# Optimization experiments

Measured on AMD Instinct MI355X. Metric: run time of the kernel, lower is better.

The kernel has to match this reference:

```python
import jax, jax.numpy as jnp
import numpy as np

B, T_IN, F, NB = 32768, 3, 6, 10
H = 256
BD = H // 2            # baseline_dim
T_OUT = 5
DIN = F + H + BD       # decoder LSTMCell input size
EPS = 1e-5


def _lstm_cell(x, h, c, W_ih, W_hh, b_ih, b_hh):
    # PyTorch gate order: i, f, g, o
    z = x @ W_ih.T + h @ W_hh.T + b_ih + b_hh
    i, f, g, o = jnp.split(z, 4, axis=-1)
    c = jax.nn.sigmoid(f) * c + jax.nn.sigmoid(i) * jnp.tanh(g)
    h = jax.nn.sigmoid(o) * jnp.tanh(c)
    return h, c


def _lstm_layer(xs, W_ih, W_hh, b_ih, b_hh):
    # xs: (T, B, D_in) -> outputs (T, B, H), final (h, c)
    Bn = xs.shape[1]
    h0 = jnp.zeros((Bn, H), xs.dtype)
    c0 = jnp.zeros((Bn, H), xs.dtype)

    def step(carry, x):
        h, c = carry
        h, c = _lstm_cell(x, h, c, W_ih, W_hh, b_ih, b_hh)
        return (h, c), h

    (hT, cT), ys = jax.lax.scan(step, (h0, c0), xs)
    return ys, hT, cT


def setup_inputs() -> dict:
    key = jax.random.key(0)
    ks = jax.random.split(key, 16)
    s = 0.05
    d = {
        "cbc_input": jax.random.normal(ks[0], (B, T_IN, F), jnp.float32),
        "baseline": jax.random.normal(ks[1], (B, NB), jnp.float32),
        # encoder LSTM layer 0 / 1
        "W_ih0": jax.random.normal(ks[2], (4 * H, F), jnp.float32) * s,
        "W_hh0": jax.random.normal(ks[3], (4 * H, H), jnp.float32) * s,
        "b_ih0": jnp.zeros((4 * H,), jnp.float32),
        "b_hh0": jnp.zeros((4 * H,), jnp.float32),
        "W_ih1": jax.random.normal(ks[4], (4 * H, H), jnp.float32) * s,
        "W_hh1": jax.random.normal(ks[5], (4 * H, H), jnp.float32) * s,
        "b_ih1": jnp.zeros((4 * H,), jnp.float32),
        "b_hh1": jnp.zeros((4 * H,), jnp.float32),
        # baseline encoder: Linear + ReLU + LayerNorm
        "Wb": jax.random.normal(ks[6], (BD, NB), jnp.float32) * s,
        "bb": jnp.zeros((BD,), jnp.float32),
        "ln_g": jnp.ones((BD,), jnp.float32),
        "ln_b": jnp.zeros((BD,), jnp.float32),
        # Bahdanau attention
        "W1a": jax.random.normal(ks[7], (H, H), jnp.float32) * s,
        "b1a": jnp.zeros((H,), jnp.float32),
        "W2a": jax.random.normal(ks[8], (H, H), jnp.float32) * s,
        "b2a": jnp.zeros((H,), jnp.float32),
        "va": jax.random.normal(ks[9], (1, H), jnp.float32) * s,
        "ba": jnp.zeros((1,), jnp.float32),
        # decoder LSTMCell
        "Wd_ih": jax.random.normal(ks[10], (4 * H, DIN), jnp.float32) * s,
        "Wd_hh": jax.random.normal(ks[11], (4 * H, H), jnp.float32) * s,
        "bd_ih": jnp.zeros((4 * H,), jnp.float32),
        "bd_hh": jnp.zeros((4 * H,), jnp.float32),
        # output projection MLP
        "Wo1": jax.random.normal(ks[12], (BD, H), jnp.float32) * s,
        "bo1": jnp.zeros((BD,), jnp.float32),
        "Wo2": jax.random.normal(ks[13], (F, BD), jnp.float32) * s,
        "bo2": jnp.zeros((F,), jnp.float32),
    }
    return d


def reference(cbc_input, baseline, W_ih0, W_hh0, b_ih0, b_hh0,
              W_ih1, W_hh1, b_ih1, b_hh1, Wb, bb, ln_g, ln_b,
              W1a, b1a, W2a, b2a, va, ba,
              Wd_ih, Wd_hh, bd_ih, bd_hh, Wo1, bo1, Wo2, bo2):
    # ---- encoder (2-layer LSTM, batch_first; eval mode so no dropout) ----
    xs = jnp.swapaxes(cbc_input, 0, 1)                      # (T, B, F)
    y0, _, _ = _lstm_layer(xs, W_ih0, W_hh0, b_ih0, b_hh0)  # (T, B, H)
    y1, hT, cT = _lstm_layer(y0, W_ih1, W_hh1, b_ih1, b_hh1)
    encoder_outputs = jnp.swapaxes(y1, 0, 1)                # (B, T, H)

    # ---- baseline encoder: Linear -> ReLU -> LayerNorm ----
    z = jax.nn.relu(baseline @ Wb.T + bb)
    mu = jnp.mean(z, axis=-1, keepdims=True)
    var = jnp.mean((z - mu) ** 2, axis=-1, keepdims=True)
    baseline_repr = (z - mu) * jax.lax.rsqrt(var + EPS) * ln_g + ln_b  # (B, BD)

    enc_proj = encoder_outputs @ W2a.T + b2a                # (B, T, H) precomputed
    last_cbc0 = cbc_input[:, -1, :]                         # (B, F)

    def step(carry, _):
        h, c, last_cbc = carry
        # Bahdanau attention
        q = (h @ W1a.T + b1a)[:, None, :]                   # (B, 1, H)
        scores = jnp.tanh(q + enc_proj) @ va.T + ba         # (B, T, 1)
        weights = jax.nn.softmax(scores, axis=1)
        context = jnp.sum(weights * encoder_outputs, axis=1)  # (B, H)
        dec_in = jnp.concatenate([last_cbc, context, baseline_repr], axis=1)
        h, c = _lstm_cell(dec_in, h, c, Wd_ih, Wd_hh, bd_ih, bd_hh)
        delta = jax.nn.relu(h @ Wo1.T + bo1) @ Wo2.T + bo2
        pred = last_cbc + delta
        return (h, c, pred), pred

    _, preds = jax.lax.scan(step, (hT, cT, last_cbc0), None, length=T_OUT)
    return jnp.swapaxes(preds, 0, 1)                        # (B, 5, F)
```

## Files before the change

kernel.cpp:

```cpp
#include <hip/hip_runtime.h>

typedef unsigned short u16;
typedef __bf16 bf16x8 __attribute__((ext_vector_type(8)));
typedef float f32x4 __attribute__((ext_vector_type(4)));

#define BATCH 32768L

__device__ __forceinline__ u16 f2b(float f) {
  union { float f; unsigned int u; } v; v.f = f;
  unsigned int r = v.u + 0x7fffu + ((v.u >> 16) & 1u);
  return (u16)(r >> 16);
}
__device__ __forceinline__ float b2f(u16 h) {
  union { unsigned int u; float f; } v; v.u = ((unsigned int)h) << 16;
  return v.f;
}
__device__ __forceinline__ float sigf(float x) { return 1.f / (1.f + __expf(-x)); }
__device__ __forceinline__ float tanh_f(float x) { return 2.f / (1.f + __expf(-2.f * x)) - 1.f; }

__device__ __forceinline__ void gload16(const void* g, void* l) {
  __builtin_amdgcn_global_load_lds((const __attribute__((address_space(1))) unsigned int*)g,
                                   (__attribute__((address_space(3))) unsigned int*)l,
                                   16, 0, 0);
}

struct PrepP {
  const float* s[9]; u16* d[9]; int sc[9]; int dc[9]; long n[9];
  const float* ba[3]; const float* bb_[3]; float* bo[3];
};

__global__ void prep_kernel(PrepP p, long cvtTotal, long total) {
  for (long i = (long)blockIdx.x * blockDim.x + threadIdx.x; i < total;
       i += (long)gridDim.x * blockDim.x) {
    if (i < cvtTotal) {
      long off = i; int sg = 0;
      while (off >= p.n[sg]) { off -= p.n[sg]; ++sg; }
      long r = off / p.dc[sg]; int c = (int)(off - r * p.dc[sg]);
      p.d[sg][off] = (c < p.sc[sg]) ? f2b(p.s[sg][r * (long)p.sc[sg] + c]) : (u16)0;
    } else {
      long j = i - cvtTotal; int sg = (int)(j >> 10); int k = (int)(j & 1023);
      p.bo[sg][k] = p.ba[sg][k] + p.bb_[sg][k];
    }
  }
}

__global__ void cvt_pad_kernel(const float* __restrict__ src, u16* __restrict__ dst,
                               long rows, int scols, int dstride) {
  long n = rows * (long)dstride;
  for (long i = (long)blockIdx.x * blockDim.x + threadIdx.x; i < n;
       i += (long)gridDim.x * blockDim.x) {
    long r = i / dstride; int c = (int)(i - r * dstride);
    dst[i] = (c < scols) ? f2b(src[r * (long)scols + c]) : (u16)0;
  }
}

__global__ void init_last_kernel(const float* __restrict__ cbc, u16* __restrict__ dec_in, long n) {
  long i = (long)blockIdx.x * 256 + threadIdx.x;
  if (i < n) {
    long r = i / 6; int j = (int)(i - r * 6);
    dec_in[r * 416 + j] = f2b(cbc[r * 18 + 12 + j]);
  }
}

__global__ void zpad_kernel(u16* __restrict__ dec_in, long n) {
  long i = (long)blockIdx.x * 256 + threadIdx.x;
  if (i < n) {
    long r = i / 26; int j = (int)(i - r * 26);
    dec_in[r * 416 + 390 + j] = 0;
  }
}

template <int EPI, int NG>
__global__ __launch_bounds__(256, 2)
void mfma_gemm3(const u16* __restrict__ A1, long lda1, int K1,
                const u16* __restrict__ W1, int wld1,
                const u16* __restrict__ A2, long lda2, int K2,
                const u16* __restrict__ W2, int wld2,
                int gs, int ys, const float* __restrict__ bias,
                u16* __restrict__ out0, int ldo, int relu,
                const float* __restrict__ cprev, float* __restrict__ cout,
                u16* __restrict__ hout, int ldh)
{
  __shared__ u16 As[2][128 * 32];
  __shared__ u16 Bs[2][NG * 64 * 32];
  const int tid = threadIdx.x;
  const int l = tid & 63, w = tid >> 6;
  const long bm = (long)blockIdx.x * 128;
  const int yb = blockIdx.y;

  const int nch1 = K1 >> 5;
  const int nch2 = A2 ? (K2 >> 5) : 0;
  const int nt = nch1 + nch2;

  f32x4 acc[8][NG];
#pragma unroll
  for (int rf = 0; rf < 8; ++rf)
#pragma unroll
    for (int g = 0; g < NG; ++g) acc[rf][g] = (f32x4){0.f, 0.f, 0.f, 0.f};

  const int l4q = l >> 2;
  const int l4r = (l & 3) * 16;

  const char* pA[2];
  const char* pB[NG];
  auto initA = [&](const u16* A, long lda) {
#pragma unroll
    for (int c = 0; c < 2; ++c)
      pA[c] = (const char*)A + ((bm + w * 32 + c * 16 + l4q) * lda) * 2 + l4r;
  };
  auto initB = [&](const u16* W, int wld) {
#pragma unroll
    for (int c = 0; c < NG; ++c) {
      const int brow = w * (NG * 16) + c * 16 + l4q;
      const long wrow = (long)(brow >> 6) * gs + (long)yb * ys + (brow & 63);
      pB[c] = (const char*)W + (wrow * (long)wld) * 2 + l4r;
    }
  };
  auto stage = [&](int buf) {
#pragma unroll
    for (int c = 0; c < 2; ++c) {
      gload16(pA[c], &As[buf][(w * 32 + c * 16) * 32]);
      pA[c] += 64;
    }
#pragma unroll
    for (int c = 0; c < NG; ++c) {
      gload16(pB[c], &Bs[buf][(w * (NG * 16) + c * 16) * 32]);
      pB[c] += 64;
    }
  };

  initA(A1, lda1);
  initB(W1, wld1);
  stage(0);
  int cur = 0;
  const int koff = (l >> 4) * 8;
  const int rb = l & 15;
  for (int ch = 0; ch < nt; ++ch) {
    if (ch + 1 == nch1 && A2) { initA(A2, lda2); initB(W2, wld2); }
    __syncthreads();
    if (ch + 1 < nt) stage(cur ^ 1);
    const u16* Ab = As[cur];
    const u16* Bb = Bs[cur];
    bf16x8 af[8];
#pragma unroll
    for (int rf = 0; rf < 8; ++rf)
      af[rf] = *(const bf16x8*)&Ab[(rf * 16 + rb) * 32 + koff];
#pragma unroll
    for (int g = 0; g < NG; ++g) {
      bf16x8 bfr = *(const bf16x8*)&Bb[(g * 64 + w * 16 + rb) * 32 + koff];
#pragma unroll
      for (int rf = 0; rf < 8; ++rf)
        acc[rf][g] = __builtin_amdgcn_mfma_f32_16x16x32_bf16(af[rf], bfr, acc[rf][g], 0, 0, 0);
    }
    cur ^= 1;
  }

  const int colb = l & 15;
  const int rq = l >> 4;
  if constexpr (EPI == 0) {
#pragma unroll
    for (int g = 0; g < NG; ++g) {
      const int wrow = g * gs + yb * ys + w * 16 + colb;
      const float bi = bias[wrow];
#pragma unroll
      for (int rf = 0; rf < 8; ++rf) {
#pragma unroll
        for (int r = 0; r < 4; ++r) {
          const long row = bm + rf * 16 + rq * 4 + r;
          float vv = acc[rf][g][r] + bi;
          if (relu) vv = fmaxf(vv, 0.f);
          out0[row * (long)ldo + wrow] = f2b(vv);
        }
      }
    }
  } else {
    const int cb = yb * 64 + w * 16 + colb;
    const float b_i = bias[cb];
    const float b_f = bias[256 + cb];
    const float b_g = bias[512 + cb];
    const float b_o = bias[768 + cb];
#pragma unroll
    for (int rf = 0; rf < 8; ++rf) {
#pragma unroll
      for (int r = 0; r < 4; ++r) {
        const long row = bm + rf * 16 + rq * 4 + r;
        const float zi = acc[rf][0][r] + b_i;
        const float zf = acc[rf][1][r] + b_f;
        const float zg = acc[rf][2][r] + b_g;
        const float zo = acc[rf][3][r] + b_o;
        const float cp = cprev ? cprev[row * 256 + cb] : 0.f;
        const float cn = sigf(zf) * cp + sigf(zi) * tanh_f(zg);
        const float hn = sigf(zo) * tanh_f(cn);
        cout[row * 256 + cb] = cn;
        hout[row * (long)ldh + cb] = f2b(hn);
      }
    }
  }
}

__global__ __launch_bounds__(256)
void baseline_kernel(const float* __restrict__ baseline, const float* __restrict__ Wb,
                     const float* __restrict__ bb, const float* __restrict__ ln_g,
                     const float* __restrict__ ln_b, u16* __restrict__ dec_in)
{
  __shared__ float wbs[1280];
  __shared__ float bbs[128], lgs[128], lbs[128];
  const int tid = threadIdx.x;
  for (int i = tid; i < 1280; i += 256) wbs[i] = Wb[i];
  if (tid < 128) { bbs[tid] = bb[tid]; lgs[tid] = ln_g[tid]; lbs[tid] = ln_b[tid]; }
  __syncthreads();
  const int l = tid & 63, w = tid >> 6;
  const long row = (long)blockIdx.x * 4 + w;
  float bl[10];
#pragma unroll
  for (int k = 0; k < 10; ++k) bl[k] = baseline[row * 10 + k];
  const int c0 = l, c1 = l + 64;
  float z0 = bbs[c0], z1 = bbs[c1];
#pragma unroll
  for (int k = 0; k < 10; ++k) { z0 += bl[k] * wbs[c0 * 10 + k]; z1 += bl[k] * wbs[c1 * 10 + k]; }
  z0 = fmaxf(z0, 0.f); z1 = fmaxf(z1, 0.f);
  float s = z0 + z1, sq = z0 * z0 + z1 * z1;
#pragma unroll
  for (int m = 32; m; m >>= 1) { s += __shfl_xor(s, m); sq += __shfl_xor(sq, m); }
  const float mu = s * (1.f / 128.f);
  const float var = sq * (1.f / 128.f) - mu * mu;
  const float rs = rsqrtf(var + 1e-5f);
  dec_in[row * 416 + 262 + c0] = f2b((z0 - mu) * rs * lgs[c0] + lbs[c0]);
  dec_in[row * 416 + 262 + c1] = f2b((z1 - mu) * rs * lgs[c1] + lbs[c1]);
}

__global__ __launch_bounds__(256)
void attn_kernel(const u16* __restrict__ q, const u16* __restrict__ ep,
                 const u16* __restrict__ eo, const float* __restrict__ va,
                 const float* __restrict__ ba, u16* __restrict__ dec_in)
{
  const int tid = threadIdx.x;
  const int l = tid & 63, w = tid >> 6;
  const long row = (long)blockIdx.x * 4 + w;
  const int c = l * 4;
  float qv[4], vav[4];
  {
    ushort4 qu = *(const ushort4*)&q[row * 256 + c];
    qv[0] = b2f(qu.x); qv[1] = b2f(qu.y); qv[2] = b2f(qu.z); qv[3] = b2f(qu.w);
    float4 vv = *(const float4*)&va[c];
    vav[0] = vv.x; vav[1] = vv.y; vav[2] = vv.z; vav[3] = vv.w;
  }
  float s[3];
#pragma unroll
  for (int t = 0; t < 3; ++t) {
    ushort4 eu = *(const ushort4*)&ep[row * 768 + t * 256 + c];
    float p = tanh_f(qv[0] + b2f(eu.x)) * vav[0]
            + tanh_f(qv[1] + b2f(eu.y)) * vav[1]
            + tanh_f(qv[2] + b2f(eu.z)) * vav[2]
            + tanh_f(qv[3] + b2f(eu.w)) * vav[3];
#pragma unroll
    for (int m = 32; m; m >>= 1) p += __shfl_xor(p, m);
    s[t] = p + ba[0];
  }
  const float mx = fmaxf(s[0], fmaxf(s[1], s[2]));
  const float e0 = __expf(s[0] - mx), e1 = __expf(s[1] - mx), e2 = __expf(s[2] - mx);
  const float inv = 1.f / (e0 + e1 + e2);
  const float w0 = e0 * inv, w1 = e1 * inv, w2 = e2 * inv;
  const ushort4 a0 = *(const ushort4*)&eo[row * 768 + 0 * 256 + c];
  const ushort4 a1 = *(const ushort4*)&eo[row * 768 + 1 * 256 + c];
  const ushort4 a2 = *(const ushort4*)&eo[row * 768 + 2 * 256 + c];
  u16* dp = &dec_in[row * 416 + 6 + c];
  dp[0] = f2b(w0 * b2f(a0.x) + w1 * b2f(a1.x) + w2 * b2f(a2.x));
  dp[1] = f2b(w0 * b2f(a0.y) + w1 * b2f(a1.y) + w2 * b2f(a2.y));
  dp[2] = f2b(w0 * b2f(a0.z) + w1 * b2f(a1.z) + w2 * b2f(a2.z));
  dp[3] = f2b(w0 * b2f(a0.w) + w1 * b2f(a1.w) + w2 * b2f(a2.w));
}

__global__ __launch_bounds__(256)
void delta_kernel(const u16* __restrict__ t1, const float* __restrict__ Wo2,
                  const float* __restrict__ bo2, const float* __restrict__ lastp, int lstride,
                  float* __restrict__ outp, int ostride, u16* __restrict__ dec_in)
{
  __shared__ float w2s[768];
  __shared__ float part[64][4][6];
  const int tid = threadIdx.x;
  for (int i = tid; i < 768; i += 256) w2s[i] = Wo2[i];
  __syncthreads();
  const int rw = tid >> 2, q = tid & 3;
  const long row = (long)blockIdx.x * 64 + rw;
  float p[6] = {0.f, 0.f, 0.f, 0.f, 0.f, 0.f};
  const u16* tp = &t1[row * 128 + q * 32];
#pragma unroll
  for (int it = 0; it < 4; ++it) {
    int4 chunk = *(const int4*)&tp[it * 8];
    const u16* cu = (const u16*)&chunk;
#pragma unroll
    for (int e = 0; e < 8; ++e) {
      const float tv = b2f(cu[e]);
      const int k = q * 32 + it * 8 + e;
#pragma unroll
      for (int j = 0; j < 6; ++j) p[j] += tv * w2s[j * 128 + k];
    }
  }
#pragma unroll
  for (int j = 0; j < 6; ++j) part[rw][q][j] = p[j];
  __syncthreads();
  if (tid < 64) {
    const long r2 = (long)blockIdx.x * 64 + tid;
#pragma unroll
    for (int j = 0; j < 6; ++j) {
      const float d = bo2[j] + part[tid][0][j] + part[tid][1][j] + part[tid][2][j] + part[tid][3][j];
      const float pr = lastp[r2 * lstride + j] + d;
      outp[r2 * ostride + j] = pr;
      dec_in[r2 * 416 + j] = f2b(pr);
    }
  }
}

extern "C" void kernel_launch(void* const* d_in, const int* in_sizes, int n_in,
                              void* d_out, int out_size, void* d_ws, size_t ws_size,
                              hipStream_t stream) {
  const float* cbc   = (const float*)d_in[0];
  const float* base  = (const float*)d_in[1];
  const float* W_ih0 = (const float*)d_in[2];
  const float* W_hh0 = (const float*)d_in[3];
  const float* b_ih0 = (const float*)d_in[4];
  const float* b_hh0 = (const float*)d_in[5];
  const float* W_ih1 = (const float*)d_in[6];
  const float* W_hh1 = (const float*)d_in[7];
  const float* b_ih1 = (const float*)d_in[8];
  const float* b_hh1 = (const float*)d_in[9];
  const float* Wb    = (const float*)d_in[10];
  const float* bb    = (const float*)d_in[11];
  const float* ln_g  = (const float*)d_in[12];
  const float* ln_b  = (const float*)d_in[13];
  const float* W1a   = (const float*)d_in[14];
  const float* b1a   = (const float*)d_in[15];
  const float* W2a   = (const float*)d_in[16];
  const float* b2a   = (const float*)d_in[17];
  const float* va    = (const float*)d_in[18];
  const float* ba    = (const float*)d_in[19];
  const float* Wd_ih = (const float*)d_in[20];
  const float* Wd_hh = (const float*)d_in[21];
  const float* bd_ih = (const float*)d_in[22];
  const float* bd_hh = (const float*)d_in[23];
  const float* Wo1   = (const float*)d_in[24];
  const float* bo1   = (const float*)d_in[25];
  const float* Wo2   = (const float*)d_in[26];
  const float* bo2   = (const float*)d_in[27];
  float* out = (float*)d_out;
  (void)in_sizes; (void)n_in; (void)out_size;

  unsigned char* wsb = (unsigned char*)d_ws;
  size_t off = 0;
  auto alloc = [&](size_t bytes) -> void* {
    void* p = wsb + off;
    off += (bytes + 255) & ~(size_t)255;
    return p;
  };
  u16* wih0b = (u16*)alloc(1024 * 32 * 2);
  u16* whh0b = (u16*)alloc(1024 * 256 * 2);
  u16* wih1b = (u16*)alloc(1024 * 256 * 2);
  u16* whh1b = (u16*)alloc(1024 * 256 * 2);
  u16* wdihb = (u16*)alloc(1024 * 416 * 2);
  u16* wdhhb = (u16*)alloc(1024 * 256 * 2);
  u16* w1ab  = (u16*)alloc(256 * 256 * 2);
  u16* w2ab  = (u16*)alloc(256 * 256 * 2);
  u16* wo1b  = (u16*)alloc(128 * 256 * 2);
  float* bsum0 = (float*)alloc(1024 * 4);
  float* bsum1 = (float*)alloc(1024 * 4);
  float* bsumd = (float*)alloc(1024 * 4);

  const long perRow = 6656;
  long avail = (long)ws_size - (long)off - 32768;
  long R = avail > 0 ? avail / perRow : 128;
  R &= ~127L;
  if (R > BATCH) R = BATCH;
  if (R < 128) R = 128;

  u16* xbf    = (u16*)alloc((size_t)R * 96 * 2);
  u16* y0     = (u16*)alloc((size_t)R * 768 * 2);
  u16* y1     = (u16*)alloc((size_t)R * 768 * 2);
  float* cbuf = (float*)alloc((size_t)R * 256 * 4);
  u16* hdec0  = (u16*)alloc((size_t)R * 256 * 2);
  u16* hdec1  = (u16*)alloc((size_t)R * 256 * 2);
  u16* qt1    = (u16*)alloc((size_t)R * 256 * 2);
  u16* dec_in = (u16*)alloc((size_t)R * 416 * 2);

  {
    PrepP p;
    const float* ss[9] = {W_ih0, W_hh0, W_ih1, W_hh1, Wd_ih, Wd_hh, W1a, W2a, Wo1};
    u16* dd[9]         = {wih0b, whh0b, wih1b, whh1b, wdihb, wdhhb, w1ab, w2ab, wo1b};
    int scv[9]         = {6, 256, 256, 256, 390, 256, 256, 256, 256};
    int dcv[9]         = {32, 256, 256, 256, 416, 256, 256, 256, 256};
    long rows[9]       = {1024, 1024, 1024, 1024, 1024, 1024, 256, 256, 128};
    long cvtTotal = 0;
    for (int i = 0; i < 9; ++i) {
      p.s[i] = ss[i]; p.d[i] = dd[i]; p.sc[i] = scv[i]; p.dc[i] = dcv[i];
      p.n[i] = rows[i] * dcv[i]; cvtTotal += p.n[i];
    }
    p.ba[0] = b_ih0; p.bb_[0] = b_hh0; p.bo[0] = bsum0;
    p.ba[1] = b_ih1; p.bb_[1] = b_hh1; p.bo[1] = bsum1;
    p.ba[2] = bd_ih; p.bb_[2] = bd_hh; p.bo[2] = bsumd;
    prep_kernel<<<dim3(2048), dim3(256), 0, stream>>>(p, cvtTotal, cvtTotal + 3072);
  }

  const dim3 blk(256);

  for (long r0 = 0; r0 < BATCH; r0 += R) {
    const long Rc = (BATCH - r0 < R) ? (BATCH - r0) : R;
    const unsigned nb = (unsigned)(Rc / 128);
    const dim3 gcell(nb, 4);
    const dim3 gfull(nb, 1);
    const float* cbc_c  = cbc + r0 * 18;
    const float* base_c = base + r0 * 10;
    float* out_c = out + r0 * 30;

    {
      long n = Rc * 3 * 32;
      long b = (n + 255) / 256; if (b > 4096) b = 4096;
      cvt_pad_kernel<<<dim3((unsigned)b), blk, 0, stream>>>(cbc_c, xbf, Rc * 3, 6, 32);
    }
    baseline_kernel<<<dim3((unsigned)(Rc / 4)), blk, 0, stream>>>(base_c, Wb, bb, ln_g, ln_b, dec_in);
    init_last_kernel<<<dim3((unsigned)((Rc * 6 + 255) / 256)), blk, 0, stream>>>(cbc_c, dec_in, Rc * 6);
    zpad_kernel<<<dim3((unsigned)((Rc * 26 + 255) / 256)), blk, 0, stream>>>(dec_in, Rc * 26);

    for (int t = 0; t < 3; ++t) {
      const u16* a2 = t ? (y0 + (t - 1) * 256) : nullptr;
      mfma_gemm3<1, 4><<<gcell, blk, 0, stream>>>(
          xbf + t * 32, 96, 32, wih0b, 32,
          a2, 768, 256, whh0b, 256,
          256, 64, bsum0,
          nullptr, 0, 0,
          (t ? cbuf : nullptr), cbuf, y0 + t * 256, 768);
    }
    for (int t = 0; t < 3; ++t) {
      const u16* a2 = t ? (y1 + (t - 1) * 256) : nullptr;
      mfma_gemm3<1, 4><<<gcell, blk, 0, stream>>>(
          y0 + t * 256, 768, 256, wih1b, 256,
          a2, 768, 256, whh1b, 256,
          256, 64, bsum1,
          nullptr, 0, 0,
          (t ? cbuf : nullptr), cbuf, y1 + t * 256, 768);
    }
    mfma_gemm3<0, 4><<<dim3(nb * 3, 1), blk, 0, stream>>>(
        y1, 256, 256, w2ab, 256,
        nullptr, 0, 0, nullptr, 0,
        64, 0, b2a,
        y0, 256, 0,
        nullptr, nullptr, nullptr, 0);

    const u16* hcur = y1 + 2 * 256; long hld = 768;
    for (int s = 0; s < 5; ++s) {
      mfma_gemm3<0, 4><<<gfull, blk, 0, stream>>>(
          hcur, hld, 256, w1ab, 256,
          nullptr, 0, 0, nullptr, 0,
          64, 0, b1a,
          qt1, 256, 0,
          nullptr, nullptr, nullptr, 0);
      attn_kernel<<<dim3((unsigned)(Rc / 4)), blk, 0, stream>>>(qt1, y0, y1, va, ba, dec_in);
      u16* hnext = (s & 1) ? hdec1 : hdec0;
      mfma_gemm3<1, 4><<<gcell, blk, 0, stream>>>(
          dec_in, 416, 416, wdihb, 416,
          hcur, hld, 256, wdhhb, 256,
          256, 64, bsumd,
          nullptr, 0, 0,
          cbuf, cbuf, hnext, 256);
      hcur = hnext; hld = 256;
      mfma_gemm3<0, 2><<<gfull, blk, 0, stream>>>(
          hcur, 256, 256, wo1b, 256,
          nullptr, 0, 0, nullptr, 0,
          64, 0, bo1,
          qt1, 128, 1,
          nullptr, nullptr, nullptr, 0);
      const float* lastp = (s == 0) ? (cbc_c + 12) : (out_c + (long)(s - 1) * 6);
      const int lstr = (s == 0) ? 18 : 30;
      delta_kernel<<<dim3((unsigned)(Rc / 64)), blk, 0, stream>>>(
          qt1, Wo2, bo2, lastp, lstr, out_c + (long)s * 6, 30, dec_in);
    }
  }
}
```

Before: 1.046 ms.

## Triple-buffer GEMM loads with swizzled LDS, fuse front kernels, split attention query GEMM

The GEMM kernel moves from two to three LDS buffers, prefetches two chunks ahead, and waits with explicit vmcnt-based waits plus a barrier so global loads overlap compute. It also XOR-swizzles the 16-byte segments in LDS to reduce bank conflicts. Four small prep kernels (input convert, last-value init, zero pad, baseline encoder) become one front kernel, and the attention query GEMM is split across two grid columns with NG=2 for more parallelism. The extra buffer raises LDS use per block, which may cut occupancy, and the hand-written waitcnt counts must match the number of loads issued per stage.

```diff
diff --git a/kernel.cpp b/kernel.cpp
--- a/kernel.cpp
+++ b/kernel.cpp
@@ -44,35 +44,9 @@
   }
 }
 
-__global__ void cvt_pad_kernel(const float* __restrict__ src, u16* __restrict__ dst,
-                               long rows, int scols, int dstride) {
-  long n = rows * (long)dstride;
-  for (long i = (long)blockIdx.x * blockDim.x + threadIdx.x; i < n;
-       i += (long)gridDim.x * blockDim.x) {
-    long r = i / dstride; int c = (int)(i - r * dstride);
-    dst[i] = (c < scols) ? f2b(src[r * (long)scols + c]) : (u16)0;
-  }
-}
-
-__global__ void init_last_kernel(const float* __restrict__ cbc, u16* __restrict__ dec_in, long n) {
-  long i = (long)blockIdx.x * 256 + threadIdx.x;
-  if (i < n) {
-    long r = i / 6; int j = (int)(i - r * 6);
-    dec_in[r * 416 + j] = f2b(cbc[r * 18 + 12 + j]);
-  }
-}
-
-__global__ void zpad_kernel(u16* __restrict__ dec_in, long n) {
-  long i = (long)blockIdx.x * 256 + threadIdx.x;
-  if (i < n) {
-    long r = i / 26; int j = (int)(i - r * 26);
-    dec_in[r * 416 + 390 + j] = 0;
-  }
-}
-
 template <int EPI, int NG>
 __global__ __launch_bounds__(256, 2)
-void mfma_gemm3(const u16* __restrict__ A1, long lda1, int K1,
+void mfma_gemm4(const u16* __restrict__ A1, long lda1, int K1,
                 const u16* __restrict__ W1, int wld1,
                 const u16* __restrict__ A2, long lda2, int K2,
                 const u16* __restrict__ W2, int wld2,
@@ -81,8 +55,8 @@
                 const float* __restrict__ cprev, float* __restrict__ cout,
                 u16* __restrict__ hout, int ldh)
 {
-  __shared__ u16 As[2][128 * 32];
-  __shared__ u16 Bs[2][NG * 64 * 32];
+  __shared__ u16 As[3][128 * 32];
+  __shared__ u16 Bs[3][NG * 64 * 32];
   const int tid = threadIdx.x;
   const int l = tid & 63, w = tid >> 6;
   const long bm = (long)blockIdx.x * 128;
@@ -99,21 +73,21 @@
     for (int g = 0; g < NG; ++g) acc[rf][g] = (f32x4){0.f, 0.f, 0.f, 0.f};
 
   const int l4q = l >> 2;
-  const int l4r = (l & 3) * 16;
+  const int swzs = ((l & 3) ^ ((l >> 2) & 3)) * 16;
 
   const char* pA[2];
   const char* pB[NG];
   auto initA = [&](const u16* A, long lda) {
 #pragma unroll
     for (int c = 0; c < 2; ++c)
-      pA[c] = (const char*)A + ((bm + w * 32 + c * 16 + l4q) * lda) * 2 + l4r;
+      pA[c] = (const char*)A + ((bm + w * 32 + c * 16 + l4q) * lda) * 2 + swzs;
   };
   auto initB = [&](const u16* W, int wld) {
 #pragma unroll
     for (int c = 0; c < NG; ++c) {
       const int brow = w * (NG * 16) + c * 16 + l4q;
       const long wrow = (long)(brow >> 6) * gs + (long)yb * ys + (brow & 63);
-      pB[c] = (const char*)W + (wrow * (long)wld) * 2 + l4r;
+      pB[c] = (const char*)W + (wrow * (long)wld) * 2 + swzs;
     }
   };
   auto stage = [&](int buf) {
@@ -132,15 +106,25 @@
   initA(A1, lda1);
   initB(W1, wld1);
   stage(0);
-  int cur = 0;
-  const int koff = (l >> 4) * 8;
+  if (A2 && nch1 == 1) { initA(A2, lda2); initB(W2, wld2); }
+  if (nt > 1) stage(1);
+
   const int rb = l & 15;
+  const int koff = ((l >> 4) ^ (l & 3)) * 8;
+  int bufR = 0, bufS = 2;
   for (int ch = 0; ch < nt; ++ch) {
-    if (ch + 1 == nch1 && A2) { initA(A2, lda2); initB(W2, wld2); }
-    __syncthreads();
-    if (ch + 1 < nt) stage(cur ^ 1);
-    const u16* Ab = As[cur];
-    const u16* Bb = Bs[cur];
+    if (ch + 1 < nt) {
+      asm volatile("s_waitcnt vmcnt(%0)\n\ts_barrier" :: "i"(2 + NG) : "memory");
+    } else {
+      asm volatile("s_waitcnt vmcnt(0)\n\ts_barrier" ::: "memory");
+    }
+    const int s = ch + 2;
+    if (s < nt) {
+      if (A2 && s == nch1) { initA(A2, lda2); initB(W2, wld2); }
+      stage(bufS);
+    }
+    const u16* Ab = As[bufR];
+    const u16* Bb = Bs[bufR];
     bf16x8 af[8];
 #pragma unroll
     for (int rf = 0; rf < 8; ++rf)
@@ -152,7 +136,8 @@
       for (int rf = 0; rf < 8; ++rf)
         acc[rf][g] = __builtin_amdgcn_mfma_f32_16x16x32_bf16(af[rf], bfr, acc[rf][g], 0, 0, 0);
     }
-    cur ^= 1;
+    bufR = (bufR == 2) ? 0 : bufR + 1;
+    bufS = (bufS == 2) ? 0 : bufS + 1;
   }
 
   const int colb = l & 15;
@@ -199,9 +184,10 @@
 }
 
 __global__ __launch_bounds__(256)
-void baseline_kernel(const float* __restrict__ baseline, const float* __restrict__ Wb,
-                     const float* __restrict__ bb, const float* __restrict__ ln_g,
-                     const float* __restrict__ ln_b, u16* __restrict__ dec_in)
+void front_kernel(const float* __restrict__ cbc, const float* __restrict__ baseline,
+                  const float* __restrict__ Wb, const float* __restrict__ bb,
+                  const float* __restrict__ ln_g, const float* __restrict__ ln_b,
+                  u16* __restrict__ dec_in, u16* __restrict__ xbf)
 {
   __shared__ float wbs[1280];
   __shared__ float bbs[128], lgs[128], lbs[128];
@@ -211,6 +197,13 @@
   __syncthreads();
   const int l = tid & 63, w = tid >> 6;
   const long row = (long)blockIdx.x * 4 + w;
+#pragma unroll
+  for (int e = l; e < 96; e += 64) {
+    const int t = e >> 5, c = e & 31;
+    xbf[(row * 3 + t) * 32 + c] = (c < 6) ? f2b(cbc[row * 18 + t * 6 + c]) : (u16)0;
+  }
+  if (l < 6) dec_in[row * 416 + l] = f2b(cbc[row * 18 + 12 + l]);
+  else if (l < 32) dec_in[row * 416 + 390 + (l - 6)] = 0;
   float bl[10];
 #pragma unroll
   for (int k = 0; k < 10; ++k) bl[k] = baseline[row * 10 + k];
@@ -406,23 +399,16 @@
     const long Rc = (BATCH - r0 < R) ? (BATCH - r0) : R;
     const unsigned nb = (unsigned)(Rc / 128);
     const dim3 gcell(nb, 4);
-    const dim3 gfull(nb, 1);
     const float* cbc_c  = cbc + r0 * 18;
     const float* base_c = base + r0 * 10;
     float* out_c = out + r0 * 30;
 
-    {
-      long n = Rc * 3 * 32;
-      long b = (n + 255) / 256; if (b > 4096) b = 4096;
-      cvt_pad_kernel<<<dim3((unsigned)b), blk, 0, stream>>>(cbc_c, xbf, Rc * 3, 6, 32);
-    }
-    baseline_kernel<<<dim3((unsigned)(Rc / 4)), blk, 0, stream>>>(base_c, Wb, bb, ln_g, ln_b, dec_in);
-    init_last_kernel<<<dim3((unsigned)((Rc * 6 + 255) / 256)), blk, 0, stream>>>(cbc_c, dec_in, Rc * 6);
-    zpad_kernel<<<dim3((unsigned)((Rc * 26 + 255) / 256)), blk, 0, stream>>>(dec_in, Rc * 26);
+    front_kernel<<<dim3((unsigned)(Rc / 4)), blk, 0, stream>>>(
+        cbc_c, base_c, Wb, bb, ln_g, ln_b, dec_in, xbf);
 
     for (int t = 0; t < 3; ++t) {
       const u16* a2 = t ? (y0 + (t - 1) * 256) : nullptr;
-      mfma_gemm3<1, 4><<<gcell, blk, 0, stream>>>(
+      mfma_gemm4<1, 4><<<gcell, blk, 0, stream>>>(
           xbf + t * 32, 96, 32, wih0b, 32,
           a2, 768, 256, whh0b, 256,
           256, 64, bsum0,
@@ -431,14 +417,14 @@
     }
     for (int t = 0; t < 3; ++t) {
       const u16* a2 = t ? (y1 + (t - 1) * 256) : nullptr;
-      mfma_gemm3<1, 4><<<gcell, blk, 0, stream>>>(
+      mfma_gemm4<1, 4><<<gcell, blk, 0, stream>>>(
           y0 + t * 256, 768, 256, wih1b, 256,
           a2, 768, 256, whh1b, 256,
           256, 64, bsum1,
           nullptr, 0, 0,
           (t ? cbuf : nullptr), cbuf, y1 + t * 256, 768);
     }
-    mfma_gemm3<0, 4><<<dim3(nb * 3, 1), blk, 0, stream>>>(
+    mfma_gemm4<0, 4><<<dim3(nb * 3, 1), blk, 0, stream>>>(
         y1, 256, 256, w2ab, 256,
         nullptr, 0, 0, nullptr, 0,
         64, 0, b2a,
@@ -447,22 +433,22 @@
 
     const u16* hcur = y1 + 2 * 256; long hld = 768;
     for (int s = 0; s < 5; ++s) {
-      mfma_gemm3<0, 4><<<gfull, blk, 0, stream>>>(
+      mfma_gemm4<0, 2><<<dim3(nb, 2), blk, 0, stream>>>(
           hcur, hld, 256, w1ab, 256,
           nullptr, 0, 0, nullptr, 0,
-          64, 0, b1a,
+          64, 128, b1a,
           qt1, 256, 0,
           nullptr, nullptr, nullptr, 0);
       attn_kernel<<<dim3((unsigned)(Rc / 4)), blk, 0, stream>>>(qt1, y0, y1, va, ba, dec_in);
       u16* hnext = (s & 1) ? hdec1 : hdec0;
-      mfma_gemm3<1, 4><<<gcell, blk, 0, stream>>>(
+      mfma_gemm4<1, 4><<<gcell, blk, 0, stream>>>(
           dec_in, 416, 416, wdihb, 416,
           hcur, hld, 256, wdhhb, 256,
           256, 64, bsumd,
           nullptr, 0, 0,
           cbuf, cbuf, hnext, 256);
       hcur = hnext; hld = 256;
-      mfma_gemm3<0, 2><<<gfull, blk, 0, stream>>>(
+      mfma_gemm4<0, 2><<<dim3(nb, 1), blk, 0, stream>>>(
           hcur, 256, 256, wo1b, 256,
           nullptr, 0, 0, nullptr, 0,
           64, 0, bo1,
```

New measurement: 1.038 ms. About the same (-0.8%).
